# Kernel tuning notes

Hardware: AMD Instinct MI355X
Metric: run time of the kernel (lower is better)

## Reference

```python
import jax, jax.numpy as jnp
import numpy as np

# LocallyConnected2D (keras, implementation=1, channels_last, valid padding, no activation)
KH, KW = 3, 3
SH, SW = 1, 1


def _extract_patches(x):
    # x: (B, H, W, C) -> patches: (B, P, KH*KW*C), flattened in (kh, kw, c) order
    B, H, W, C = x.shape
    out_h = (H - KH) // SH + 1
    out_w = (W - KW) // SW + 1
    i_idx = (jnp.arange(out_h) * SH)[:, None] + jnp.arange(KH)  # (out_h, KH)
    j_idx = (jnp.arange(out_w) * SW)[:, None] + jnp.arange(KW)  # (out_w, KW)
    p = x[:, i_idx]              # (B, out_h, KH, W, C)
    p = p[:, :, :, j_idx]        # (B, out_h, KH, out_w, KW, C)
    p = p.transpose(0, 1, 3, 2, 4, 5)  # (B, out_h, out_w, KH, KW, C)
    return p.reshape(B, out_h * out_w, KH * KW * C), out_h, out_w


def setup_inputs() -> dict:
    key = jax.random.key(0)
    k1, k2, k3 = jax.random.split(key, 3)
    B, H, W, C = 16, 64, 64, 32
    out_h = (H - KH) // SH + 1
    out_w = (W - KW) // SW + 1
    P = out_h * out_w            # 3844
    K = KH * KW * C              # 288
    F = 64
    x = jax.random.normal(k1, (B, H, W, C), dtype=jnp.float32)
    kernel = jax.random.normal(k2, (P, K, F), dtype=jnp.float32) * 0.05
    bias = jax.random.normal(k3, (P, F), dtype=jnp.float32) * 0.05
    return {"x": x, "kernel": kernel, "bias": bias}


def reference(x, kernel, bias):
    B = x.shape[0]
    patches, out_h, out_w = _extract_patches(x)      # (B, P, K)
    # per-location unshared matmul: each spatial location p has its own (K, F) kernel
    out = jnp.einsum('bpk,pkf->bpf', patches, kernel) + bias[None]  # (B, P, F)
    return out.reshape(B, out_h, out_w, -1)
```

## Files before the change

### kernel.cpp

```cpp
#include <hip/hip_runtime.h>


typedef _Float16 f16x4 __attribute__((ext_vector_type(4)));
typedef float    f32x4 __attribute__((ext_vector_type(4)));

namespace {
constexpr int Wc = 64, Cc = 32;
constexpr int OWc = 62;
constexpr int Pc  = 3844;
constexpr int Fc  = 64;
constexpr int KFc = 288 * 64;
constexpr size_t XB = (size_t)64 * 64 * 32;
}

#define BTILE(ACC, T)                                                       \
    {                                                                       \
        const float* wb = wh + (T) * 16;                                    \
        f16x4 bf;                                                           \
        bf[0] = (_Float16)wb[0 * Fc];                                       \
        bf[1] = (_Float16)wb[1 * Fc];                                       \
        bf[2] = (_Float16)wb[2 * Fc];                                       \
        bf[3] = (_Float16)wb[3 * Fc];                                       \
        ACC = __builtin_amdgcn_mfma_f32_16x16x16f16(a, bf, ACC, 0, 0, 0);   \
    }

__global__ __launch_bounds__(256)
void lc2d(const float* __restrict__ x, const float* __restrict__ kern,
          const float* __restrict__ bias, float* __restrict__ out)
{
    const int t    = threadIdx.x;
    const int lane = t & 63;
    const int wid  = t >> 6;
    const int lq   = lane & 15;
    const int lg   = lane >> 4;

    const int p  = blockIdx.x * 4 + wid;
    const int oh = p / OWc;
    const int ow = p - oh * OWc;

    const float* xlane = x + (size_t)lq * XB + ((size_t)oh * Wc + ow) * Cc + 4 * lg;
    const float* wlane = kern + (size_t)p * KFc + (size_t)(4 * lg) * Fc + lq;

    f32x4 acc0 = {0.f, 0.f, 0.f, 0.f};
    f32x4 acc1 = {0.f, 0.f, 0.f, 0.f};
    f32x4 acc2 = {0.f, 0.f, 0.f, 0.f};
    f32x4 acc3 = {0.f, 0.f, 0.f, 0.f};

    for (int pos = 0; pos < 9; ++pos) {
        const int kh = (pos * 11) >> 5;
        const int kw = pos - kh * 3;
        const float* xp = xlane + (size_t)(kh * Wc + kw) * Cc;
        const float* wp = wlane + (size_t)(pos * 32) * Fc;

        const float4 xa0 = *(const float4*)(xp);
        const float4 xa1 = *(const float4*)(xp + 16);
        f16x4 a0, a1;
        a0[0] = (_Float16)xa0.x; a0[1] = (_Float16)xa0.y;
        a0[2] = (_Float16)xa0.z; a0[3] = (_Float16)xa0.w;
        a1[0] = (_Float16)xa1.x; a1[1] = (_Float16)xa1.y;
        a1[2] = (_Float16)xa1.z; a1[3] = (_Float16)xa1.w;

        {
            const float* wh = wp;
            const f16x4 a = a0;
            BTILE(acc0, 0) BTILE(acc1, 1) BTILE(acc2, 2) BTILE(acc3, 3)
        }
        {
            const float* wh = wp + 16 * Fc;
            const f16x4 a = a1;
            BTILE(acc0, 0) BTILE(acc1, 1) BTILE(acc2, 2) BTILE(acc3, 3)
        }
    }

    const float b0 = bias[(size_t)p * Fc +  0 + lq];
    const float b1 = bias[(size_t)p * Fc + 16 + lq];
    const float b2 = bias[(size_t)p * Fc + 32 + lq];
    const float b3 = bias[(size_t)p * Fc + 48 + lq];
    #pragma unroll
    for (int r = 0; r < 4; ++r) {
        float* o = out + ((size_t)(4 * lg + r) * Pc + p) * Fc + lq;
        o[ 0] = acc0[r] + b0;
        o[16] = acc1[r] + b1;
        o[32] = acc2[r] + b2;
        o[48] = acc3[r] + b3;
    }
}

extern "C" void kernel_launch(void* const* d_in, const int* in_sizes, int n_in,
                              void* d_out, int out_size, void* d_ws, size_t ws_size,
                              hipStream_t stream)
{
    const float* x    = (const float*)d_in[0];
    const float* kern = (const float*)d_in[1];
    const float* bias = (const float*)d_in[2];
    float* out = (float*)d_out;
    dim3 grid(Pc / 4);
    lc2d<<<grid, 256, 0, stream>>>(x, kern, bias, out);
}
```

Baseline: 55.30 us.

## Stream per-location weights through double-buffered LDS via direct global-to-LDS loads

Weights are now copied into a per-wave double buffer in LDS with `global_load_lds`, 16 bytes per lane and fully coalesced. The 288x64 weight matrix is split into 18 stages of 16 rows, and the next stage is prefetched while the current one is computed. Manual `vmcnt` and `lgkmcnt` waits plus scheduling barriers enforce the ordering. The goal is to replace strided 4-byte global reads with wide coalesced transfers and to overlap memory with MFMA work. The trade-offs are extra LDS traffic and reliance on hand-written wait counts. The `x` load issued inside the compute step may force the compiler to drain the prefetch queue, which would cancel the overlap.

```diff
diff --git a/kernel.cpp b/kernel.cpp
--- a/kernel.cpp
+++ b/kernel.cpp
@@ -13,64 +13,94 @@
 constexpr size_t XB = (size_t)64 * 64 * 32;
 }
 
-#define BTILE(ACC, T)                                                       \
-    {                                                                       \
-        const float* wb = wh + (T) * 16;                                    \
-        f16x4 bf;                                                           \
-        bf[0] = (_Float16)wb[0 * Fc];                                       \
-        bf[1] = (_Float16)wb[1 * Fc];                                       \
-        bf[2] = (_Float16)wb[2 * Fc];                                       \
-        bf[3] = (_Float16)wb[3 * Fc];                                       \
-        ACC = __builtin_amdgcn_mfma_f32_16x16x16f16(a, bf, ACC, 0, 0, 0);   \
-    }
+#define GLD_LDS(gp, lp)                                                        \
+    __builtin_amdgcn_global_load_lds(                                          \
+        (const __attribute__((address_space(1))) void*)(gp),                   \
+        (__attribute__((address_space(3))) void*)(lp), 16, 0, 0)
 
 __global__ __launch_bounds__(256)
 void lc2d(const float* __restrict__ x, const float* __restrict__ kern,
           const float* __restrict__ bias, float* __restrict__ out)
 {
+    __shared__ float wl[4][2][1024];
+
     const int t    = threadIdx.x;
     const int lane = t & 63;
-    const int wid  = t >> 6;
+    const int wv   = t >> 6;
     const int lq   = lane & 15;
     const int lg   = lane >> 4;
 
-    const int p  = blockIdx.x * 4 + wid;
+    const int p  = blockIdx.x * 4 + wv;
     const int oh = p / OWc;
     const int ow = p - oh * OWc;
 
+    const float* kp    = kern + (size_t)p * KFc;
     const float* xlane = x + (size_t)lq * XB + ((size_t)oh * Wc + ow) * Cc + 4 * lg;
-    const float* wlane = kern + (size_t)p * KFc + (size_t)(4 * lg) * Fc + lq;
 
-    f32x4 acc0 = {0.f, 0.f, 0.f, 0.f};
-    f32x4 acc1 = {0.f, 0.f, 0.f, 0.f};
-    f32x4 acc2 = {0.f, 0.f, 0.f, 0.f};
-    f32x4 acc3 = {0.f, 0.f, 0.f, 0.f};
+    f32x4 acc0 = {0.f,0.f,0.f,0.f}, acc1 = {0.f,0.f,0.f,0.f};
+    f32x4 acc2 = {0.f,0.f,0.f,0.f}, acc3 = {0.f,0.f,0.f,0.f};
 
-    for (int pos = 0; pos < 9; ++pos) {
-        const int kh = (pos * 11) >> 5;
-        const int kw = pos - kh * 3;
-        const float* xp = xlane + (size_t)(kh * Wc + kw) * Cc;
-        const float* wp = wlane + (size_t)(pos * 32) * Fc;
+    #define ISSUE(s, b)                                                        \
+    {                                                                          \
+        const float* g_ = kp + (size_t)(s) * 1024 + lane * 4;                  \
+        GLD_LDS(g_ + 0 * 256, &wl[wv][(b)][0 * 256]);                          \
+        GLD_LDS(g_ + 1 * 256, &wl[wv][(b)][1 * 256]);                          \
+        GLD_LDS(g_ + 2 * 256, &wl[wv][(b)][2 * 256]);                          \
+        GLD_LDS(g_ + 3 * 256, &wl[wv][(b)][3 * 256]);                          \
+    }
 
-        const float4 xa0 = *(const float4*)(xp);
-        const float4 xa1 = *(const float4*)(xp + 16);
-        f16x4 a0, a1;
-        a0[0] = (_Float16)xa0.x; a0[1] = (_Float16)xa0.y;
-        a0[2] = (_Float16)xa0.z; a0[3] = (_Float16)xa0.w;
-        a1[0] = (_Float16)xa1.x; a1[1] = (_Float16)xa1.y;
-        a1[2] = (_Float16)xa1.z; a1[3] = (_Float16)xa1.w;
+    #define COMPUTE(s, b)                                                      \
+    {                                                                          \
+        const int pos_  = (s) >> 1;                                            \
+        const int half_ = (s) & 1;                                             \
+        const int kh_   = (pos_ * 11) >> 5;              \
+        const int kw_   = pos_ - kh_ * 3;                                      \
+        const float4 xa_ = *(const float4*)(xlane                              \
+                              + (size_t)(kh_ * Wc + kw_) * Cc + half_ * 16);   \
+        f16x4 a_;                                                              \
+        a_[0] = (_Float16)xa_.x; a_[1] = (_Float16)xa_.y;                      \
+        a_[2] = (_Float16)xa_.z; a_[3] = (_Float16)xa_.w;                      \
+        const float* r_ = &wl[wv][(b)][(4 * lg) * 64 + lq];                    \
+        {                                                                      \
+            f16x4 bf_;                                                         \
+            bf_[0]=(_Float16)r_[ 0+  0]; bf_[1]=(_Float16)r_[ 0+ 64];          \
+            bf_[2]=(_Float16)r_[ 0+128]; bf_[3]=(_Float16)r_[ 0+192];          \
+            acc0 = __builtin_amdgcn_mfma_f32_16x16x16f16(a_, bf_, acc0, 0,0,0);\
+        }                                                                      \
+        {                                                                      \
+            f16x4 bf_;                                                         \
+            bf_[0]=(_Float16)r_[16+  0]; bf_[1]=(_Float16)r_[16+ 64];          \
+            bf_[2]=(_Float16)r_[16+128]; bf_[3]=(_Float16)r_[16+192];          \
+            acc1 = __builtin_amdgcn_mfma_f32_16x16x16f16(a_, bf_, acc1, 0,0,0);\
+        }                                                                      \
+        {                                                                      \
+            f16x4 bf_;                                                         \
+            bf_[0]=(_Float16)r_[32+  0]; bf_[1]=(_Float16)r_[32+ 64];          \
+            bf_[2]=(_Float16)r_[32+128]; bf_[3]=(_Float16)r_[32+192];          \
+            acc2 = __builtin_amdgcn_mfma_f32_16x16x16f16(a_, bf_, acc2, 0,0,0);\
+        }                                                                      \
+        {                                                                      \
+            f16x4 bf_;                                                         \
+            bf_[0]=(_Float16)r_[48+  0]; bf_[1]=(_Float16)r_[48+ 64];          \
+            bf_[2]=(_Float16)r_[48+128]; bf_[3]=(_Float16)r_[48+192];          \
+            acc3 = __builtin_amdgcn_mfma_f32_16x16x16f16(a_, bf_, acc3, 0,0,0);\
+        }                                                                      \
+    }
 
-        {
-            const float* wh = wp;
-            const f16x4 a = a0;
-            BTILE(acc0, 0) BTILE(acc1, 1) BTILE(acc2, 2) BTILE(acc3, 3)
-        }
-        {
-            const float* wh = wp + 16 * Fc;
-            const f16x4 a = a1;
-            BTILE(acc0, 0) BTILE(acc1, 1) BTILE(acc2, 2) BTILE(acc3, 3)
-        }
+    ISSUE(0, 0)
+    ISSUE(1, 1)
+
+    for (int s = 0; s < 17; ++s) {
+        asm volatile("s_waitcnt vmcnt(4)" ::: "memory");
+        __builtin_amdgcn_sched_barrier(0);
+        COMPUTE(s, s & 1)
+        asm volatile("s_waitcnt lgkmcnt(0)" ::: "memory");
+        __builtin_amdgcn_sched_barrier(0);
+        if (s < 16) ISSUE(s + 2, s & 1)
     }
+    asm volatile("s_waitcnt vmcnt(0)" ::: "memory");
+    __builtin_amdgcn_sched_barrier(0);
+    COMPUTE(17, 1)
 
     const float b0 = bias[(size_t)p * Fc +  0 + lq];
     const float b1 = bias[(size_t)p * Fc + 16 + lq];
```

Result: slower. 57.25 us (+3.5%).
